# Kernel optimization log

Hardware: AMD Instinct MI355X
Metric: run time of the kernel (lower is better)

The kernel has to match this reference:

```python
import jax, jax.numpy as jnp
import numpy as np

EPS = 1e-5

def conv2d(x, w, padding):
    # x: (N, Cin, H, W), w: (Cout, Cin, kh, kw)
    return jax.lax.conv_general_dilated(
        x, w, window_strides=(1, 1),
        padding=[(padding, padding), (padding, padding)],
        dimension_numbers=('NCHW', 'OIHW', 'NCHW'))

def proj_bn_relu(x, w, gamma, beta, mean, var):
    # 1x1 conv + BatchNorm (eval mode, running stats) + ReLU
    y = conv2d(x, w, 0)
    scale = (gamma / jnp.sqrt(var + EPS))[None, :, None, None]
    shift = (beta - mean * gamma / jnp.sqrt(var + EPS))[None, :, None, None]
    return jax.nn.relu(y * scale + shift)

def setup_inputs() -> dict:
    key = jax.random.key(0)
    ks = jax.random.split(key, 16)
    B, Sx, Sy, C1, C2, Co, H, W, K = 2, 4, 4, 64, 64, 64, 128, 128, 3
    inp = {
        'u': jax.random.normal(ks[0], (B, Sx, C1, H, W), jnp.float32),
        'v': jax.random.normal(ks[1], (B, Sy, C2, H, W), jnp.float32),
        'pu_w': jax.random.normal(ks[2], (C1, C1, 1, 1), jnp.float32) * 0.05,
        'pu_gamma': jnp.ones((C1,), jnp.float32),
        'pu_beta': jnp.zeros((C1,), jnp.float32),
        'pu_mean': jax.random.normal(ks[3], (C1,), jnp.float32) * 0.1,
        'pu_var': jax.random.uniform(ks[4], (C1,), jnp.float32, 0.5, 1.5),
        'pv_w': jax.random.normal(ks[5], (C2, C2, 1, 1), jnp.float32) * 0.05,
        'pv_gamma': jnp.ones((C2,), jnp.float32),
        'pv_beta': jnp.zeros((C2,), jnp.float32),
        'pv_mean': jax.random.normal(ks[6], (C2,), jnp.float32) * 0.1,
        'pv_var': jax.random.uniform(ks[7], (C2,), jnp.float32, 0.5, 1.5),
        'conv_w': jax.random.normal(ks[8], (Co, C1 + C2, K, K), jnp.float32) * 0.02,
        'conv_b': jax.random.normal(ks[9], (Co,), jnp.float32) * 0.02,
    }
    return inp

def reference(u, v, pu_w, pu_gamma, pu_beta, pu_mean, pu_var,
              pv_w, pv_gamma, pv_beta, pv_mean, pv_var, conv_w, conv_b):
    B, Sx, C1, H, W = u.shape
    _, Sy, C2, _, _ = v.shape
    pad = 1
    # flatten set dims into batch for the 1x1 proj+BN+ReLU
    uf = proj_bn_relu(u.reshape(B * Sx, C1, H, W), pu_w, pu_gamma, pu_beta, pu_mean, pu_var)
    vf = proj_bn_relu(v.reshape(B * Sy, C2, H, W), pv_w, pv_gamma, pv_beta, pv_mean, pv_var)
    # conv over concat channels is linear -> split weight and broadcast-add,
    # exactly equal to conv(cat(repeat(u), repeat(v))) without materializing
    # the (B,Sx,Sy,C1+C2,H,W) tensor.
    w_u = conv_w[:, :C1]   # (Co, C1, K, K)
    w_v = conv_w[:, C1:]   # (Co, C2, K, K)
    ou = conv2d(uf, w_u, pad)  # (B*Sx, Co, Ho, Wo)
    ov = conv2d(vf, w_v, pad)  # (B*Sy, Co, Ho, Wo)
    Co, Ho, Wo = ou.shape[1], ou.shape[2], ou.shape[3]
    ou = ou.reshape(B, Sx, 1, Co, Ho, Wo)
    ov = ov.reshape(B, 1, Sy, Co, Ho, Wo)
    out = ou + ov + conv_b[None, None, None, :, None, None]
    return out  # (B, Sx, Sy, Co, Ho, Wo)
```

## Files before the change

### kernel.cpp

```cpp
#include <hip/hip_runtime.h>
#include <hip/hip_bf16.h>

#define C   64
#define Hh  128
#define Ww  128
#define HW  16384

typedef __attribute__((ext_vector_type(8))) short bf16x8;
typedef __attribute__((ext_vector_type(4))) float f32x4;

__device__ __forceinline__ unsigned short f2bf(float f) {
    unsigned u = __builtin_bit_cast(unsigned, f);
    unsigned r = (u + 0x7fff + ((u >> 16) & 1)) >> 16;
    return (unsigned short)r;
}

__global__ __launch_bounds__(256) void prep_kernel(
    const float* __restrict__ pu_w, const float* __restrict__ pu_g,
    const float* __restrict__ pu_b, const float* __restrict__ pu_m,
    const float* __restrict__ pu_v,
    const float* __restrict__ pv_w, const float* __restrict__ pv_g,
    const float* __restrict__ pv_b, const float* __restrict__ pv_m,
    const float* __restrict__ pv_v,
    const float* __restrict__ conv_w,
    short* __restrict__ pwu, short* __restrict__ pwv,
    short* __restrict__ wpu, short* __restrict__ wpv,
    float* __restrict__ shu, float* __restrict__ shv)
{
    const int idx = blockIdx.x * 256 + threadIdx.x;
    if (idx < 8192) {
        const int c  = idx >> 12;
        const int r  = idx & 4095;
        const int co = r >> 6, ci = r & 63;
        const float* w = c ? pv_w : pu_w;
        const float* g = c ? pv_g : pu_g;
        const float* vv = c ? pv_v : pu_v;
        const float scale = g[co] * rsqrtf(vv[co] + 1e-5f);
        (c ? pwv : pwu)[r] = (short)f2bf(w[co * 64 + ci] * scale);
    } else if (idx < 81920) {
        const int flat = idx - 8192;
        const int c  = flat / 36864;
        const int r  = flat % 36864;
        const int ch  = r / 18432;
        const int r2  = r % 18432;
        const int tap = r2 / 2048;
        const int r3  = r2 & 2047;
        const int co = r3 >> 5, ci = r3 & 31;
        const float src = conv_w[(size_t)(co * 128 + c * 64 + ch * 32 + ci) * 9 + tap];
        (c ? wpv : wpu)[((ch * 9 + tap) * 64 + co) * 32 + ci] = (short)f2bf(src);
    } else if (idx < 82048) {
        const int r  = idx - 81920;
        const int c  = r >> 6, co = r & 63;
        const float* g = c ? pv_g : pu_g;
        const float* b = c ? pv_b : pu_b;
        const float* m = c ? pv_m : pu_m;
        const float* vv = c ? pv_v : pu_v;
        const float scale = g[co] * rsqrtf(vv[co] + 1e-5f);
        (c ? shv : shu)[co] = b[co] - m[co] * scale;
    }
}

__global__ __launch_bounds__(256) void proj_mfma(
    const float* __restrict__ x, const short* __restrict__ pw,
    const float* __restrict__ shiftg, short* __restrict__ y)
{
    __shared__ short xs[256 * 72];
    __shared__ short pwl[64 * 72];
    __shared__ float ssh[64];

    const int img  = blockIdx.y;
    const int pix0 = blockIdx.x * 256;
    const int tid  = threadIdx.x;

    const float* xi = x + (size_t)img * C * HW + pix0 + tid;
#pragma unroll 8
    for (int c2 = 0; c2 < 32; ++c2) {
        const float a = xi[(size_t)(2 * c2) * HW];
        const float b = xi[(size_t)(2 * c2 + 1) * HW];
        const int packed = (int)f2bf(a) | ((int)f2bf(b) << 16);
        *(int*)(&xs[tid * 72 + c2 * 2]) = packed;
    }
#pragma unroll
    for (int it = 0; it < 2; ++it) {
        const int idx = tid + it * 256;
        const int oct = idx & 7, co = idx >> 3;
        *(int4*)(&pwl[co * 72 + oct * 8]) = *(const int4*)(&pw[co * 64 + oct * 8]);
    }
    if (tid < 64) ssh[tid] = shiftg[tid];
    __syncthreads();

    const int wq = tid >> 6;
    const int lane = tid & 63;
    const int lx = lane & 15;
    const int q  = lane >> 4;

    f32x4 acc[4][4];
#pragma unroll
    for (int mt = 0; mt < 4; ++mt)
#pragma unroll
        for (int nt = 0; nt < 4; ++nt) acc[mt][nt] = (f32x4){0.f, 0.f, 0.f, 0.f};

#pragma unroll
    for (int kc = 0; kc < 2; ++kc) {
        bf16x8 a[4], b[4];
#pragma unroll
        for (int mt = 0; mt < 4; ++mt)
            a[mt] = *(const bf16x8*)&xs[((wq * 4 + mt) * 16 + lx) * 72 + kc * 32 + q * 8];
#pragma unroll
        for (int nt = 0; nt < 4; ++nt)
            b[nt] = *(const bf16x8*)&pwl[(nt * 16 + lx) * 72 + kc * 32 + q * 8];
#pragma unroll
        for (int mt = 0; mt < 4; ++mt)
#pragma unroll
            for (int nt = 0; nt < 4; ++nt)
                acc[mt][nt] = __builtin_amdgcn_mfma_f32_16x16x32_bf16(a[mt], b[nt], acc[mt][nt], 0, 0, 0);
    }

    short* yo = y + ((size_t)img * HW + pix0) * C;
#pragma unroll
    for (int mt = 0; mt < 4; ++mt)
#pragma unroll
        for (int nt = 0; nt < 4; ++nt)
#pragma unroll
            for (int r = 0; r < 4; ++r) {
                const int pixl = (wq * 4 + mt) * 16 + q * 4 + r;
                const int co = nt * 16 + lx;
                float vv = acc[mt][nt][r] + ssh[co];
                vv = fmaxf(vv, 0.f);
                yo[(size_t)pixl * C + co] = (short)f2bf(vv);
            }
}

__global__ __launch_bounds__(256, 2) void conv_mfma(
    const short* __restrict__ uf, const short* __restrict__ wp,
    float* __restrict__ out)
{
    __shared__ short xs[340 * 40];
    __shared__ short wsm[5 * 64 * 40];

    const int img = blockIdx.y;
    const int tx = blockIdx.x & 3, ty = blockIdx.x >> 2;
    const int h0 = ty * 8, w0 = tx * 32;
    const int tid = threadIdx.x;
    const int wq = tid >> 6;
    const int lane = tid & 63;
    const int lx = lane & 15;
    const int q8 = (lane >> 4) * 8;

    f32x4 acc[4][4];
#pragma unroll
    for (int mt = 0; mt < 4; ++mt)
#pragma unroll
        for (int nt = 0; nt < 4; ++nt) acc[mt][nt] = (f32x4){0.f, 0.f, 0.f, 0.f};

    const short* ub = uf + (size_t)img * HW * C;

    for (int ch = 0; ch < 2; ++ch) {
        __syncthreads();
        for (int idx = tid; idx < 1360; idx += 256) {
            const int oct = idx & 3;
            const int pcell = idx >> 2;
            const int h = pcell / 34, w = pcell - h * 34;
            const int gh = h0 - 1 + h, gw = w0 - 1 + w;
            int4 v = {0, 0, 0, 0};
            if (gh >= 0 && gh < Hh && gw >= 0 && gw < Ww)
                v = *(const int4*)&ub[(size_t)(gh * Ww + gw) * C + ch * 32 + oct * 8];
            *(int4*)(&xs[pcell * 40 + oct * 8]) = v;
        }
        for (int tg = 0; tg < 2; ++tg) {
            const int tb = tg ? 5 : 0;
            const int ntap = tg ? 4 : 5;
            if (tg) __syncthreads();
            for (int idx = tid; idx < ntap * 256; idx += 256) {
                const int oct = idx & 3;
                const int co = (idx >> 2) & 63;
                const int tl = idx >> 8;
                *(int4*)(&wsm[(tl * 64 + co) * 40 + oct * 8]) =
                    *(const int4*)&wp[(((ch * 9 + tb + tl) * 64) + co) * 32 + oct * 8];
            }
            __syncthreads();
            for (int tl = 0; tl < ntap; ++tl) {
                const int t = tb + tl;
                const int ky = (t < 3) ? 0 : ((t < 6) ? 1 : 2);
                const int kx = t - ky * 3;
                bf16x8 a[4], b[4];
#pragma unroll
                for (int mt = 0; mt < 4; ++mt)
                    a[mt] = *(const bf16x8*)&wsm[(tl * 64 + mt * 16 + lx) * 40 + q8];
#pragma unroll
                for (int nt = 0; nt < 4; ++nt) {
                    const int cell = (2 * wq + (nt >> 1) + ky) * 34 + (nt & 1) * 16 + lx + kx;
                    b[nt] = *(const bf16x8*)&xs[cell * 40 + q8];
                }
#pragma unroll
                for (int mt = 0; mt < 4; ++mt)
#pragma unroll
                    for (int nt = 0; nt < 4; ++nt)
                        acc[mt][nt] = __builtin_amdgcn_mfma_f32_16x16x32_bf16(a[mt], b[nt], acc[mt][nt], 0, 0, 0);
            }
        }
    }

    const int qq = lane >> 4;
    float* ob = out + (size_t)img * C * HW;
#pragma unroll
    for (int mt = 0; mt < 4; ++mt)
#pragma unroll
        for (int nt = 0; nt < 4; ++nt)
#pragma unroll
            for (int r = 0; r < 4; ++r) {
                const int co = mt * 16 + qq * 4 + r;
                const int h = h0 + 2 * wq + (nt >> 1);
                const int w = w0 + (nt & 1) * 16 + lx;
                ob[(size_t)co * HW + h * Ww + w] = acc[mt][nt][r];
            }
}

__global__ __launch_bounds__(256) void addb_kernel(
    const float* __restrict__ ou, const float* __restrict__ ov,
    const float* __restrict__ bias, float* __restrict__ out)
{
    const size_t i4 = (size_t)blockIdx.x * 256 + threadIdx.x;
    const int    hw4 = (int)(i4 & 4095);
    const size_t q   = i4 >> 12;
    const int co = (int)(q & 63);
    const size_t p = q >> 6;
    const int sy = (int)(p & 3);
    const int sx = (int)((p >> 2) & 3);
    const int b  = (int)(p >> 4);

    const float4 o1 = ((const float4*)ou)[((size_t)(b * 4 + sx) * C + co) * 4096 + hw4];
    const float4 o2 = ((const float4*)ov)[((size_t)(b * 4 + sy) * C + co) * 4096 + hw4];
    const float bb = bias[co];
    float4 r;
    r.x = o1.x + o2.x + bb;
    r.y = o1.y + o2.y + bb;
    r.z = o1.z + o2.z + bb;
    r.w = o1.w + o2.w + bb;
    ((float4*)out)[i4] = r;
}

extern "C" void kernel_launch(void* const* d_in, const int* in_sizes, int n_in,
                              void* d_out, int out_size, void* d_ws, size_t ws_size,
                              hipStream_t stream)
{
    const float* u        = (const float*)d_in[0];
    const float* v        = (const float*)d_in[1];
    const float* pu_w     = (const float*)d_in[2];
    const float* pu_gamma = (const float*)d_in[3];
    const float* pu_beta  = (const float*)d_in[4];
    const float* pu_mean  = (const float*)d_in[5];
    const float* pu_var   = (const float*)d_in[6];
    const float* pv_w     = (const float*)d_in[7];
    const float* pv_gamma = (const float*)d_in[8];
    const float* pv_beta  = (const float*)d_in[9];
    const float* pv_mean  = (const float*)d_in[10];
    const float* pv_var   = (const float*)d_in[11];
    const float* conv_w   = (const float*)d_in[12];
    const float* conv_b   = (const float*)d_in[13];
    float* out = (float*)d_out;

    char* ws = (char*)d_ws;
    short* uf  = (short*)(ws);
    short* vf  = (short*)(ws + 16777216);
    float* ou  = (float*)(ws + 33554432);
    float* ov  = (float*)(ws + 67108864);
    char*  aux = ws + 100663296;
    short* pwu = (short*)(aux);
    short* pwv = (short*)(aux + 8192);
    short* wpu = (short*)(aux + 16384);
    short* wpv = (short*)(aux + 90112);
    float* shu = (float*)(aux + 163840);
    float* shv = (float*)(aux + 164096);

    prep_kernel<<<321, 256, 0, stream>>>(pu_w, pu_gamma, pu_beta, pu_mean, pu_var,
                                         pv_w, pv_gamma, pv_beta, pv_mean, pv_var,
                                         conv_w, pwu, pwv, wpu, wpv, shu, shv);

    dim3 gp(64, 8);
    proj_mfma<<<gp, 256, 0, stream>>>(u, pwu, shu, uf);
    proj_mfma<<<gp, 256, 0, stream>>>(v, pwv, shv, vf);

    dim3 gc(64, 8);
    conv_mfma<<<gc, 256, 0, stream>>>(uf, wpu, ou);
    conv_mfma<<<gc, 256, 0, stream>>>(vf, wpv, ov);

    const size_t n4 = (size_t)out_size / 4;
    addb_kernel<<<(unsigned)(n4 / 256), 256, 0, stream>>>(ou, ov, conv_b, out);
}
```

Baseline: 281.6 us.

## Fuse broadcast-add into v-conv epilogue and merge projection launches

The separate add-bias kernel is removed. The v-branch conv now adds the bias and the u-branch conv result directly in its epilogue, writing the four sx outputs with nontemporal stores, so the ov intermediate is never written or re-read. The two projection launches are merged into one grid over both inputs, and all nine weight taps are staged in LDS at once, which drops a barrier but raises shared-memory use. The fused epilogue reads ou four times per tile and issues scattered stores, which may limit occupancy or store efficiency.

```diff
diff --git a/kernel.cpp b/kernel.cpp
--- a/kernel.cpp
+++ b/kernel.cpp
@@ -61,14 +61,23 @@
 }
 
 __global__ __launch_bounds__(256) void proj_mfma(
-    const float* __restrict__ x, const short* __restrict__ pw,
-    const float* __restrict__ shiftg, short* __restrict__ y)
+    const float* __restrict__ xu, const float* __restrict__ xv,
+    const short* __restrict__ pwu_, const short* __restrict__ pwv_,
+    const float* __restrict__ shu_, const float* __restrict__ shv_,
+    short* __restrict__ yu, short* __restrict__ yv)
 {
     __shared__ short xs[256 * 72];
     __shared__ short pwl[64 * 72];
     __shared__ float ssh[64];
 
-    const int img  = blockIdx.y;
+    const int img16 = blockIdx.y;
+    const int sel   = img16 >> 3;
+    const int img   = img16 & 7;
+    const float* x      = sel ? xv   : xu;
+    const short* pw     = sel ? pwv_ : pwu_;
+    const float* shiftg = sel ? shv_ : shu_;
+    short* y            = sel ? yv   : yu;
+
     const int pix0 = blockIdx.x * 256;
     const int tid  = threadIdx.x;
 
@@ -131,12 +140,15 @@
             }
 }
 
-__global__ __launch_bounds__(256, 2) void conv_mfma(
-    const short* __restrict__ uf, const short* __restrict__ wp,
-    float* __restrict__ out)
+template<bool FUSED>
+__global__ __launch_bounds__(256, 2) void conv_core(
+    const short* __restrict__ act, const short* __restrict__ wp,
+    const float* __restrict__ ou, const float* __restrict__ bias,
+    float* __restrict__ outp)
 {
     __shared__ short xs[340 * 40];
-    __shared__ short wsm[5 * 64 * 40];
+    __shared__ short wsm[9 * 64 * 40];
+    __shared__ float sbias[64];
 
     const int img = blockIdx.y;
     const int tx = blockIdx.x & 3, ty = blockIdx.x >> 2;
@@ -147,13 +159,15 @@
     const int lx = lane & 15;
     const int q8 = (lane >> 4) * 8;
 
+    if (FUSED && tid < 64) sbias[tid] = bias[tid];
+
     f32x4 acc[4][4];
 #pragma unroll
     for (int mt = 0; mt < 4; ++mt)
 #pragma unroll
         for (int nt = 0; nt < 4; ++nt) acc[mt][nt] = (f32x4){0.f, 0.f, 0.f, 0.f};
 
-    const short* ub = uf + (size_t)img * HW * C;
+    const short* ub = act + (size_t)img * HW * C;
 
     for (int ch = 0; ch < 2; ++ch) {
         __syncthreads();
@@ -167,77 +181,78 @@
                 v = *(const int4*)&ub[(size_t)(gh * Ww + gw) * C + ch * 32 + oct * 8];
             *(int4*)(&xs[pcell * 40 + oct * 8]) = v;
         }
-        for (int tg = 0; tg < 2; ++tg) {
-            const int tb = tg ? 5 : 0;
-            const int ntap = tg ? 4 : 5;
-            if (tg) __syncthreads();
-            for (int idx = tid; idx < ntap * 256; idx += 256) {
-                const int oct = idx & 3;
-                const int co = (idx >> 2) & 63;
-                const int tl = idx >> 8;
-                *(int4*)(&wsm[(tl * 64 + co) * 40 + oct * 8]) =
-                    *(const int4*)&wp[(((ch * 9 + tb + tl) * 64) + co) * 32 + oct * 8];
+        for (int idx = tid; idx < 2304; idx += 256) {
+            const int oct = idx & 3;
+            const int co = (idx >> 2) & 63;
+            const int tl = idx >> 8;
+            *(int4*)(&wsm[(tl * 64 + co) * 40 + oct * 8]) =
+                *(const int4*)&wp[(((ch * 9 + tl) * 64) + co) * 32 + oct * 8];
+        }
+        __syncthreads();
+#pragma unroll
+        for (int t = 0; t < 9; ++t) {
+            const int ky = t / 3;
+            const int kx = t - ky * 3;
+            bf16x8 a[4], b[4];
+#pragma unroll
+            for (int mt = 0; mt < 4; ++mt)
+                a[mt] = *(const bf16x8*)&wsm[(t * 64 + mt * 16 + lx) * 40 + q8];
+#pragma unroll
+            for (int nt = 0; nt < 4; ++nt) {
+                const int cell = (2 * wq + (nt >> 1) + ky) * 34 + (nt & 1) * 16 + lx + kx;
+                b[nt] = *(const bf16x8*)&xs[cell * 40 + q8];
             }
-            __syncthreads();
-            for (int tl = 0; tl < ntap; ++tl) {
-                const int t = tb + tl;
-                const int ky = (t < 3) ? 0 : ((t < 6) ? 1 : 2);
-                const int kx = t - ky * 3;
-                bf16x8 a[4], b[4];
-#pragma unroll
-                for (int mt = 0; mt < 4; ++mt)
-                    a[mt] = *(const bf16x8*)&wsm[(tl * 64 + mt * 16 + lx) * 40 + q8];
-#pragma unroll
-                for (int nt = 0; nt < 4; ++nt) {
-                    const int cell = (2 * wq + (nt >> 1) + ky) * 34 + (nt & 1) * 16 + lx + kx;
-                    b[nt] = *(const bf16x8*)&xs[cell * 40 + q8];
+#pragma unroll
+            for (int mt = 0; mt < 4; ++mt)
+#pragma unroll
+                for (int nt = 0; nt < 4; ++nt)
+                    acc[mt][nt] = __builtin_amdgcn_mfma_f32_16x16x32_bf16(a[mt], b[nt], acc[mt][nt], 0, 0, 0);
+        }
+    }
+
+    const int qq = lane >> 4;
+    if (!FUSED) {
+        float* ob = outp + (size_t)img * C * HW;
+#pragma unroll
+        for (int mt = 0; mt < 4; ++mt)
+#pragma unroll
+            for (int nt = 0; nt < 4; ++nt)
+#pragma unroll
+                for (int r = 0; r < 4; ++r) {
+                    const int co = mt * 16 + qq * 4 + r;
+                    const int h = h0 + 2 * wq + (nt >> 1);
+                    const int w = w0 + (nt & 1) * 16 + lx;
+                    ob[(size_t)co * HW + h * Ww + w] = acc[mt][nt][r];
                 }
-#pragma unroll
-                for (int mt = 0; mt < 4; ++mt)
-#pragma unroll
-                    for (int nt = 0; nt < 4; ++nt)
-                        acc[mt][nt] = __builtin_amdgcn_mfma_f32_16x16x32_bf16(a[mt], b[nt], acc[mt][nt], 0, 0, 0);
-            }
+    } else {
+        const int b  = img >> 2;
+        const int sy = img & 3;
+#pragma unroll
+        for (int mt = 0; mt < 4; ++mt)
+#pragma unroll
+            for (int nt = 0; nt < 4; ++nt)
+#pragma unroll
+                for (int r = 0; r < 4; ++r)
+                    acc[mt][nt][r] += sbias[mt * 16 + qq * 4 + r];
+
+#pragma unroll
+        for (int sx = 0; sx < 4; ++sx) {
+            const float* oub = ou + (size_t)(b * 4 + sx) * C * HW;
+            float* ob = outp + ((size_t)((b * 4 + sx) * 4 + sy)) * C * HW;
+#pragma unroll
+            for (int mt = 0; mt < 4; ++mt)
+#pragma unroll
+                for (int nt = 0; nt < 4; ++nt)
+#pragma unroll
+                    for (int r = 0; r < 4; ++r) {
+                        const int co = mt * 16 + qq * 4 + r;
+                        const int h = h0 + 2 * wq + (nt >> 1);
+                        const int w = w0 + (nt & 1) * 16 + lx;
+                        const size_t off = (size_t)co * HW + h * Ww + w;
+                        __builtin_nontemporal_store(acc[mt][nt][r] + oub[off], &ob[off]);
+                    }
         }
     }
-
-    const int qq = lane >> 4;
-    float* ob = out + (size_t)img * C * HW;
-#pragma unroll
-    for (int mt = 0; mt < 4; ++mt)
-#pragma unroll
-        for (int nt = 0; nt < 4; ++nt)
-#pragma unroll
-            for (int r = 0; r < 4; ++r) {
-                const int co = mt * 16 + qq * 4 + r;
-                const int h = h0 + 2 * wq + (nt >> 1);
-                const int w = w0 + (nt & 1) * 16 + lx;
-                ob[(size_t)co * HW + h * Ww + w] = acc[mt][nt][r];
-            }
-}
-
-__global__ __launch_bounds__(256) void addb_kernel(
-    const float* __restrict__ ou, const float* __restrict__ ov,
-    const float* __restrict__ bias, float* __restrict__ out)
-{
-    const size_t i4 = (size_t)blockIdx.x * 256 + threadIdx.x;
-    const int    hw4 = (int)(i4 & 4095);
-    const size_t q   = i4 >> 12;
-    const int co = (int)(q & 63);
-    const size_t p = q >> 6;
-    const int sy = (int)(p & 3);
-    const int sx = (int)((p >> 2) & 3);
-    const int b  = (int)(p >> 4);
-
-    const float4 o1 = ((const float4*)ou)[((size_t)(b * 4 + sx) * C + co) * 4096 + hw4];
-    const float4 o2 = ((const float4*)ov)[((size_t)(b * 4 + sy) * C + co) * 4096 + hw4];
-    const float bb = bias[co];
-    float4 r;
-    r.x = o1.x + o2.x + bb;
-    r.y = o1.y + o2.y + bb;
-    r.z = o1.z + o2.z + bb;
-    r.w = o1.w + o2.w + bb;
-    ((float4*)out)[i4] = r;
 }
 
 extern "C" void kernel_launch(void* const* d_in, const int* in_sizes, int n_in,
@@ -264,7 +279,6 @@
     short* uf  = (short*)(ws);
     short* vf  = (short*)(ws + 16777216);
     float* ou  = (float*)(ws + 33554432);
-    float* ov  = (float*)(ws + 67108864);
     char*  aux = ws + 100663296;
     short* pwu = (short*)(aux);
     short* pwv = (short*)(aux + 8192);
@@ -277,14 +291,10 @@
                                          pv_w, pv_gamma, pv_beta, pv_mean, pv_var,
                                          conv_w, pwu, pwv, wpu, wpv, shu, shv);
 
-    dim3 gp(64, 8);
-    proj_mfma<<<gp, 256, 0, stream>>>(u, pwu, shu, uf);
-    proj_mfma<<<gp, 256, 0, stream>>>(v, pwv, shv, vf);
+    dim3 gp(64, 16);
+    proj_mfma<<<gp, 256, 0, stream>>>(u, v, pwu, pwv, shu, shv, uf, vf);
 
     dim3 gc(64, 8);
-    conv_mfma<<<gc, 256, 0, stream>>>(uf, wpu, ou);
-    conv_mfma<<<gc, 256, 0, stream>>>(vf, wpv, ov);
-
-    const size_t n4 = (size_t)out_size / 4;
-    addb_kernel<<<(unsigned)(n4 / 256), 256, 0, stream>>>(ou, ov, conv_b, out);
-}
+    conv_core<false><<<gc, 256, 0, stream>>>(uf, wpu, nullptr, nullptr, ou);
+    conv_core<true ><<<gc, 256, 0, stream>>>(vf, wpv, ou, conv_b, out);
+}
```

Result: faster. 262.7 us (-6.7%).
